# Performance work log

Measured on AMD Instinct MI355X. Metric: run time of the kernel, lower is better.

The kernel has to match this reference:

```python
import jax, jax.numpy as jnp
import numpy as np

K_NEIGHBORS = 16
HEADS = 4
BN_EPS = 1e-5


def _bn(x, p):
    # eval-mode BatchNorm; p is [4, C] = (gamma, beta, running_mean, running_var), x is [..., C]
    g, b, m, v = p[0], p[1], p[2], p[3]
    return (x - m) * (g / jnp.sqrt(v + BN_EPS)) + b


def setup_inputs() -> dict:
    key = jax.random.key(0)
    ks = jax.random.split(key, 16)
    B, C, H, W = 4, 192, 32, 32
    Hd = 384  # hidden_channels

    def bn_params(k, c):
        k1, k2, k3, k4 = jax.random.split(k, 4)
        gamma = 1.0 + 0.1 * jax.random.normal(k1, (c,), jnp.float32)
        beta = 0.1 * jax.random.normal(k2, (c,), jnp.float32)
        mean = 0.1 * jax.random.normal(k3, (c,), jnp.float32)
        var = jax.random.uniform(k4, (c,), jnp.float32, 0.5, 1.5)
        return jnp.stack([gamma, beta, mean, var])

    x = jax.random.normal(ks[0], (B, C, H, W), jnp.float32)
    W1 = 0.05 * jax.random.normal(ks[1], (C, C), jnp.float32)          # fc1 1x1 conv [out,in]
    b1 = 0.02 * jax.random.normal(ks[2], (C,), jnp.float32)
    bn1 = bn_params(ks[3], C)
    Wg = 0.05 * jax.random.normal(ks[4], (C, HEADS * Hd), jnp.float32)  # GATConv shared lin
    att_src = 0.1 * jax.random.normal(ks[5], (HEADS, Hd), jnp.float32)
    att_dst = 0.1 * jax.random.normal(ks[6], (HEADS, Hd), jnp.float32)
    bg = 0.02 * jax.random.normal(ks[7], (Hd,), jnp.float32)            # GATConv bias (concat=False)
    bng = bn_params(ks[8], Hd)
    W2 = 0.05 * jax.random.normal(ks[9], (C, Hd), jnp.float32)          # fc2 1x1 conv [out,in]
    b2 = 0.02 * jax.random.normal(ks[10], (C,), jnp.float32)
    bn2 = bn_params(ks[11], C)
    return {"x": x, "W1": W1, "b1": b1, "bn1": bn1, "Wg": Wg,
            "att_src": att_src, "att_dst": att_dst, "bg": bg, "bng": bng,
            "W2": W2, "b2": b2, "bn2": bn2}


def reference(x, W1, b1, bn1, Wg, att_src, att_dst, bg, bng, W2, b2, bn2):
    B, C, H, W = x.shape
    N = H * W
    Hd = Wg.shape[1] // HEADS
    xf = x.reshape(B, C, N).transpose(0, 2, 1)          # [B,N,C] node features
    shortcut = xf

    # fc1: 1x1 conv + BN
    y = _bn(xf @ W1.T + b1, bn1)                        # [B,N,C]

    # dynamic KNN graph per image (loop=True -> self included, distance 0)
    sq = jnp.sum(y * y, axis=-1)                        # [B,N]
    dist = sq[:, :, None] + sq[:, None, :] - 2.0 * jnp.einsum('bnc,bmc->bnm', y, y)
    idx = jax.lax.top_k(-dist, K_NEIGHBORS)[1]          # [B,N,k] neighbor (source) ids
    bidx = jnp.arange(B)[:, None, None]

    # GATConv (shared lin, heads=4, concat=False -> mean over heads)
    h = (y @ Wg).reshape(B, N, HEADS, Hd)               # [B,N,h,d]
    a_src = jnp.sum(h * att_src, axis=-1)               # [B,N,h]
    a_dst = jnp.sum(h * att_dst, axis=-1)               # [B,N,h]
    e = jax.nn.leaky_relu(a_src[bidx, idx] + a_dst[:, :, None, :], 0.2)  # [B,N,k,h]
    attn = jax.nn.softmax(e, axis=2)                    # softmax over the k incoming edges
    h_nbr = h[bidx, idx]                                # [B,N,k,h,d] gathered neighbor feats
    g = jnp.einsum('bnkh,bnkhd->bnhd', attn, h_nbr).mean(axis=2) + bg  # [B,N,Hd]

    g = jax.nn.gelu(_bn(g, bng), approximate=False)

    # fc2: 1x1 conv + BN, residual
    out = _bn(g @ W2.T + b2, bn2) + shortcut            # [B,N,C]
    return out.transpose(0, 2, 1).reshape(B, C, H, W)
```

## Files before the change

### kernel.cpp

```cpp
#include <hip/hip_runtime.h>
#include <math.h>

#define Bb 4
#define Cc 192
#define NN 1024
#define HD 384
#define NH 4
#define FF 1536
#define KN 16
#define BN_EPS 1e-5f

typedef __attribute__((ext_vector_type(8))) short bf16x8;
typedef __attribute__((ext_vector_type(4))) float f32x4;

__device__ inline float b2f(ushort u) {
  return __uint_as_float(((unsigned)u) << 16);
}
__device__ inline ushort f2b(float f) {
  unsigned v = __float_as_uint(f);
  return (ushort)((v + 0x7fffu + ((v >> 16) & 1u)) >> 16);
}

#define FMA_ROW(ACC, AV, B) \
  ACC.x = fmaf(AV, B.x, ACC.x); ACC.y = fmaf(AV, B.y, ACC.y); \
  ACC.z = fmaf(AV, B.z, ACC.z); ACC.w = fmaf(AV, B.w, ACC.w);

__global__ __launch_bounds__(256) void k_prep(
    const float* __restrict__ W1, const float* __restrict__ W2,
    const float* __restrict__ Wg, float* __restrict__ W1T,
    ushort* __restrict__ W2b, ushort* __restrict__ WgTb) {
  __shared__ float tile[32][33];
  int id = blockIdx.x;
  int t = threadIdx.x;
  if (id < 36 || id >= 108) {
    const float* in; int R, C, cx, cy;
    float* outf = nullptr; ushort* outb = nullptr;
    if (id < 36) { in = W1; R = Cc; C = Cc; cx = id % 6; cy = id / 6; outf = W1T; }
    else { int q = id - 108; in = Wg; R = Cc; C = FF; cx = q % 48; cy = q / 48; outb = WgTb; }
    int c0 = cx * 32, r0 = cy * 32;
    int tx = t & 31, ty = t >> 5;
#pragma unroll
    for (int i = 0; i < 4; ++i) {
      int r = ty + i * 8;
      tile[r][tx] = in[(size_t)(r0 + r) * C + c0 + tx];
    }
    __syncthreads();
#pragma unroll
    for (int i = 0; i < 4; ++i) {
      int r = ty + i * 8;
      float v = tile[tx][r];
      if (outf) outf[(size_t)(c0 + r) * R + r0 + tx] = v;
      else      outb[(size_t)(c0 + r) * R + r0 + tx] = f2b(v);
    }
  } else {
    int base = (id - 36) * 1024 + t * 4;
    float4 v = *(const float4*)&W2[base];
    ushort4 o = {f2b(v.x), f2b(v.y), f2b(v.z), f2b(v.w)};
    *(ushort4*)&W2b[base] = o;
  }
}

__global__ __launch_bounds__(256) void k_fc1(
    const float* __restrict__ x, const float* __restrict__ W1T,
    const float* __restrict__ b1, const float* __restrict__ bn1,
    float* __restrict__ y, ushort* __restrict__ yb,
    float* __restrict__ yT) {
  int nt = blockIdx.x, ct = blockIdx.y, b = blockIdx.z;
  int n0 = nt * 64, ct64 = ct * 64;
  __shared__ float As[64][64];
  __shared__ float Bs[64][64];
  __shared__ float ctile[64][68];
  int t = threadIdx.x;
  int tx = t & 15, ty = t >> 4;
  float4 acc[4];
#pragma unroll
  for (int i = 0; i < 4; ++i) acc[i] = {0.f, 0.f, 0.f, 0.f};
  for (int k0 = 0; k0 < Cc; k0 += 64) {
    __syncthreads();
#pragma unroll
    for (int i = 0; i < 4; ++i) {
      int fi = i * 256 + t;
      int r = fi >> 4, q = fi & 15;
      *(float4*)&As[r][q * 4] =
          *(const float4*)&x[((size_t)b * Cc + k0 + r) * NN + n0 + q * 4];
      *(float4*)&Bs[r][q * 4] =
          *(const float4*)&W1T[(size_t)(k0 + r) * Cc + ct64 + q * 4];
    }
    __syncthreads();
#pragma unroll 8
    for (int k = 0; k < 64; ++k) {
      float4 a = *(const float4*)&As[k][ty * 4];
      float4 bv = *(const float4*)&Bs[k][tx * 4];
      FMA_ROW(acc[0], a.x, bv)
      FMA_ROW(acc[1], a.y, bv)
      FMA_ROW(acc[2], a.z, bv)
      FMA_ROW(acc[3], a.w, bv)
    }
  }
  float s[4], mm[4], be[4], bias[4];
#pragma unroll
  for (int jj = 0; jj < 4; ++jj) {
    int c = ct64 + tx * 4 + jj;
    s[jj]    = bn1[c] / sqrtf(bn1[3 * Cc + c] + BN_EPS);
    mm[jj]   = bn1[2 * Cc + c];
    be[jj]   = bn1[Cc + c];
    bias[jj] = b1[c];
  }
  float accm[4][4] = {
      {acc[0].x, acc[0].y, acc[0].z, acc[0].w},
      {acc[1].x, acc[1].y, acc[1].z, acc[1].w},
      {acc[2].x, acc[2].y, acc[2].z, acc[2].w},
      {acc[3].x, acc[3].y, acc[3].z, acc[3].w}};
#pragma unroll
  for (int ii = 0; ii < 4; ++ii) {
    int n = n0 + ty * 4 + ii;
    float4 o;
    o.x = (accm[ii][0] + bias[0] - mm[0]) * s[0] + be[0];
    o.y = (accm[ii][1] + bias[1] - mm[1]) * s[1] + be[1];
    o.z = (accm[ii][2] + bias[2] - mm[2]) * s[2] + be[2];
    o.w = (accm[ii][3] + bias[3] - mm[3]) * s[3] + be[3];
    *(float4*)&y[((size_t)b * NN + n) * Cc + ct64 + tx * 4] = o;
    ushort4 ob = {f2b(o.x), f2b(o.y), f2b(o.z), f2b(o.w)};
    *(ushort4*)&yb[((size_t)b * NN + n) * Cc + ct64 + tx * 4] = ob;
    ctile[tx * 4 + 0][ty * 4 + ii] = o.x;
    ctile[tx * 4 + 1][ty * 4 + ii] = o.y;
    ctile[tx * 4 + 2][ty * 4 + ii] = o.z;
    ctile[tx * 4 + 3][ty * 4 + ii] = o.w;
  }
  __syncthreads();
#pragma unroll
  for (int i = 0; i < 4; ++i) {
    int u = i * 256 + t;
    int cl = u >> 4, q = u & 15;
    float4 v = *(const float4*)&ctile[cl][q * 4];
    *(float4*)&yT[((size_t)b * Cc + ct64 + cl) * NN + n0 + q * 4] = v;
  }
}

__global__ __launch_bounds__(64) void k_sq(const float* __restrict__ y,
                                           float* __restrict__ sq) {
  int bn = blockIdx.x;
  int lane = threadIdx.x;
  const float* yp = y + (size_t)bn * Cc;
  float s = 0.f;
  for (int k = lane; k < Cc; k += 64) { float v = yp[k]; s = fmaf(v, v, s); }
#pragma unroll
  for (int off = 32; off; off >>= 1) s += __shfl_down(s, off);
  if (lane == 0) sq[bn] = s;
}

__global__ __launch_bounds__(256) void k_hgemm_mfma(
    const ushort* __restrict__ yb, const ushort* __restrict__ WgTb,
    ushort* __restrict__ hb) {
  int r0 = blockIdx.x * 128, c0 = blockIdx.y * 128;
  __shared__ ushort Al[128][72];
  __shared__ ushort Bl[128][72];
  int t = threadIdx.x;
  int w = t >> 6, l = t & 63;
  int wr = w >> 1, wc = w & 1;
  f32x4 acc[4][4];
#pragma unroll
  for (int mt = 0; mt < 4; ++mt)
#pragma unroll
    for (int nt = 0; nt < 4; ++nt) acc[mt][nt] = {0.f, 0.f, 0.f, 0.f};
  for (int k0 = 0; k0 < Cc; k0 += 64) {
    __syncthreads();
#pragma unroll
    for (int i = 0; i < 4; ++i) {
      int u = i * 256 + t;
      int r = u >> 3, ko = (u & 7) * 8;
      *(int4*)&Al[r][ko] = *(const int4*)&yb[(size_t)(r0 + r) * Cc + k0 + ko];
      *(int4*)&Bl[r][ko] = *(const int4*)&WgTb[(size_t)(c0 + r) * Cc + k0 + ko];
    }
    __syncthreads();
#pragma unroll
    for (int ks = 0; ks < 2; ++ks) {
      bf16x8 af[4], bfr[4];
#pragma unroll
      for (int mt = 0; mt < 4; ++mt)
        af[mt] = *(const bf16x8*)&Al[wr * 64 + mt * 16 + (l & 15)][ks * 32 + (l >> 4) * 8];
#pragma unroll
      for (int nt = 0; nt < 4; ++nt)
        bfr[nt] = *(const bf16x8*)&Bl[wc * 64 + nt * 16 + (l & 15)][ks * 32 + (l >> 4) * 8];
#pragma unroll
      for (int mt = 0; mt < 4; ++mt)
#pragma unroll
        for (int nt = 0; nt < 4; ++nt)
          acc[mt][nt] = __builtin_amdgcn_mfma_f32_16x16x32_bf16(
              af[mt], bfr[nt], acc[mt][nt], 0, 0, 0);
    }
  }
  int col_l = l & 15, rg = l >> 4;
#pragma unroll
  for (int mt = 0; mt < 4; ++mt)
#pragma unroll
    for (int nt = 0; nt < 4; ++nt) {
      int col = c0 + wc * 64 + nt * 16 + col_l;
#pragma unroll
      for (int j = 0; j < 4; ++j) {
        int row = r0 + wr * 64 + mt * 16 + rg * 4 + j;
        hb[(size_t)row * FF + col] = f2b(acc[mt][nt][j]);
      }
    }
}

__global__ __launch_bounds__(256) void k_attn_coef(
    const ushort* __restrict__ hb, const float* __restrict__ att_src,
    const float* __restrict__ att_dst, float* __restrict__ asrc,
    float* __restrict__ adst) {
  int bn = blockIdx.x;
  int head = threadIdx.x / 64, lane = threadIdx.x % 64;
  const ushort* hp = hb + (size_t)bn * FF + head * HD;
  const float* as = att_src + head * HD;
  const float* ad = att_dst + head * HD;
  float s1 = 0.f, s2 = 0.f;
  for (int d = lane; d < HD; d += 64) {
    float v = b2f(hp[d]);
    s1 = fmaf(v, as[d], s1);
    s2 = fmaf(v, ad[d], s2);
  }
#pragma unroll
  for (int off = 32; off; off >>= 1) {
    s1 += __shfl_down(s1, off);
    s2 += __shfl_down(s2, off);
  }
  if (lane == 0) {
    asrc[bn * NH + head] = s1;
    adst[bn * NH + head] = s2;
  }
}

__global__ __launch_bounds__(256) void k_dist(const float* __restrict__ yT,
                                              const float* __restrict__ sq,
                                              float* __restrict__ dist) {
  int b = blockIdx.z;
  int n0 = blockIdx.y * 128, m0 = blockIdx.x * 64;
  __shared__ float As[64][128];
  __shared__ float Bs[64][64];
  const float* ytb = yT + (size_t)b * Cc * NN;
  int t = threadIdx.x;
  int tx = t & 15, ty = t >> 4;
  float4 acc[8];
#pragma unroll
  for (int i = 0; i < 8; ++i) acc[i] = {0.f, 0.f, 0.f, 0.f};
  for (int k0 = 0; k0 < Cc; k0 += 64) {
    __syncthreads();
#pragma unroll
    for (int i = 0; i < 8; ++i) {
      int fi = i * 256 + t;
      int kk = fi >> 5, n4 = fi & 31;
      *(float4*)&As[kk][n4 * 4] =
          *(const float4*)&ytb[(size_t)(k0 + kk) * NN + n0 + n4 * 4];
    }
#pragma unroll
    for (int i = 0; i < 4; ++i) {
      int fi = i * 256 + t;
      int kk = fi >> 4, m4 = fi & 15;
      *(float4*)&Bs[kk][m4 * 4] =
          *(const float4*)&ytb[(size_t)(k0 + kk) * NN + m0 + m4 * 4];
    }
    __syncthreads();
#pragma unroll 8
    for (int k = 0; k < 64; ++k) {
      float4 a0 = *(const float4*)&As[k][ty * 4];
      float4 a1 = *(const float4*)&As[k][64 + ty * 4];
      float4 b4 = *(const float4*)&Bs[k][tx * 4];
      FMA_ROW(acc[0], a0.x, b4)
      FMA_ROW(acc[1], a0.y, b4)
      FMA_ROW(acc[2], a0.z, b4)
      FMA_ROW(acc[3], a0.w, b4)
      FMA_ROW(acc[4], a1.x, b4)
      FMA_ROW(acc[5], a1.y, b4)
      FMA_ROW(acc[6], a1.z, b4)
      FMA_ROW(acc[7], a1.w, b4)
    }
  }
#pragma unroll
  for (int ii = 0; ii < 8; ++ii) {
    int n = n0 + ((ii < 4) ? (ty * 4 + ii) : (64 + ty * 4 + ii - 4));
    float sn = sq[b * NN + n];
    int mbase = m0 + tx * 4;
    float av[4] = {acc[ii].x, acc[ii].y, acc[ii].z, acc[ii].w};
    float4 o;
    o.x = sn + sq[b * NN + mbase + 0] - 2.f * av[0];
    o.y = sn + sq[b * NN + mbase + 1] - 2.f * av[1];
    o.z = sn + sq[b * NN + mbase + 2] - 2.f * av[2];
    o.w = sn + sq[b * NN + mbase + 3] - 2.f * av[3];
    *(float4*)&dist[((size_t)b * NN + n) * NN + mbase] = o;
  }
}

__global__ __launch_bounds__(64) void k_topk(const float* __restrict__ dist,
                                             int* __restrict__ idx) {
  int bn = blockIdx.x;
  int lane = threadIdx.x;
  const float4* dp = (const float4*)(dist + (size_t)bn * NN);
  float dv[16];
#pragma unroll
  for (int q = 0; q < 4; ++q) {
    float4 v = dp[lane + 64 * q];
    dv[q * 4 + 0] = v.x; dv[q * 4 + 1] = v.y;
    dv[q * 4 + 2] = v.z; dv[q * 4 + 3] = v.w;
  }
  for (int sel = 0; sel < KN; ++sel) {
    float bv = INFINITY;
    int bi = 0x7fffffff;
#pragma unroll
    for (int q = 0; q < 4; ++q)
#pragma unroll
      for (int j = 0; j < 4; ++j) {
        int m = (lane + 64 * q) * 4 + j;
        float v = dv[q * 4 + j];
        if (v < bv || (v == bv && m < bi)) { bv = v; bi = m; }
      }
#pragma unroll
    for (int off = 32; off; off >>= 1) {
      float ov = __shfl_xor(bv, off);
      int oi   = __shfl_xor(bi, off);
      if (ov < bv || (ov == bv && oi < bi)) { bv = ov; bi = oi; }
    }
    if (lane == 0) idx[bn * KN + sel] = bi;
#pragma unroll
    for (int q = 0; q < 4; ++q)
#pragma unroll
      for (int j = 0; j < 4; ++j)
        if ((lane + 64 * q) * 4 + j == bi) dv[q * 4 + j] = INFINITY;
  }
}

__global__ __launch_bounds__(128, 4) void k_gat(
    const ushort* __restrict__ hb, const float* __restrict__ asrc,
    const float* __restrict__ adst, const int* __restrict__ idx,
    const float* __restrict__ bg, const float* __restrict__ bng,
    ushort* __restrict__ gb) {
  int bid = blockIdx.x;
  int bn = (bid & 7) * (Bb * NN / 8) + (bid >> 3);
  int b = bn / NN;
  __shared__ int nb[KN];
  __shared__ float attn[KN][NH];
  int t = threadIdx.x;
  if (t < KN) nb[t] = idx[bn * KN + t];
  __syncthreads();
  if (t < KN * NH) {
    int k = t % KN, hd = t / KN;
    float e = asrc[((size_t)b * NN + nb[k]) * NH + hd] +
              adst[(size_t)bn * NH + hd];
    e = (e >= 0.f) ? e : 0.2f * e;
    attn[k][hd] = e;
  }
  __syncthreads();
  if (t < NH) {
    float mx = -INFINITY;
    for (int k = 0; k < KN; ++k) mx = fmaxf(mx, attn[k][t]);
    float s = 0.f;
    for (int k = 0; k < KN; ++k) {
      float ev = expf(attn[k][t] - mx);
      attn[k][t] = ev;
      s += ev;
    }
    float inv = 1.f / s;
    for (int k = 0; k < KN; ++k) attn[k][t] *= inv;
  }
  __syncthreads();
  if (t < 96) {
    int d = t * 4;
    float4 acc = {0.f, 0.f, 0.f, 0.f};
#pragma unroll 4
    for (int k = 0; k < KN; ++k) {
      const ushort* hp = hb + ((size_t)b * NN + nb[k]) * FF + d;
      float4 aw = *(const float4*)&attn[k][0];
      ushort4 u0 = *(const ushort4*)&hp[0];
      ushort4 u1 = *(const ushort4*)&hp[HD];
      ushort4 u2 = *(const ushort4*)&hp[2 * HD];
      ushort4 u3 = *(const ushort4*)&hp[3 * HD];
      float4 h0 = {b2f(u0.x), b2f(u0.y), b2f(u0.z), b2f(u0.w)};
      float4 h1 = {b2f(u1.x), b2f(u1.y), b2f(u1.z), b2f(u1.w)};
      float4 h2 = {b2f(u2.x), b2f(u2.y), b2f(u2.z), b2f(u2.w)};
      float4 h3 = {b2f(u3.x), b2f(u3.y), b2f(u3.z), b2f(u3.w)};
      acc.x = fmaf(aw.x, h0.x, acc.x); acc.x = fmaf(aw.y, h1.x, acc.x);
      acc.x = fmaf(aw.z, h2.x, acc.x); acc.x = fmaf(aw.w, h3.x, acc.x);
      acc.y = fmaf(aw.x, h0.y, acc.y); acc.y = fmaf(aw.y, h1.y, acc.y);
      acc.y = fmaf(aw.z, h2.y, acc.y); acc.y = fmaf(aw.w, h3.y, acc.y);
      acc.z = fmaf(aw.x, h0.z, acc.z); acc.z = fmaf(aw.y, h1.z, acc.z);
      acc.z = fmaf(aw.z, h2.z, acc.z); acc.z = fmaf(aw.w, h3.z, acc.z);
      acc.w = fmaf(aw.x, h0.w, acc.w); acc.w = fmaf(aw.y, h1.w, acc.w);
      acc.w = fmaf(aw.z, h2.w, acc.w); acc.w = fmaf(aw.w, h3.w, acc.w);
    }
    float o[4] = {acc.x, acc.y, acc.z, acc.w};
    ushort4 r;
    ushort* rp = (ushort*)&r;
#pragma unroll
    for (int j = 0; j < 4; ++j) {
      int dd = d + j;
      float val = o[j] * 0.25f + bg[dd];
      float sc = bng[dd] / sqrtf(bng[3 * HD + dd] + BN_EPS);
      val = (val - bng[2 * HD + dd]) * sc + bng[HD + dd];
      val = 0.5f * val * (1.f + erff(val * 0.7071067811865475f));
      rp[j] = f2b(val);
    }
    *(ushort4*)&gb[(size_t)bn * HD + d] = r;
  }
}

__global__ __launch_bounds__(256) void k_fc2_mfma(
    const ushort* __restrict__ gb, const ushort* __restrict__ W2b,
    const float* __restrict__ b2, const float* __restrict__ bn2,
    const float* __restrict__ x, float* __restrict__ out) {
  int r0 = blockIdx.x * 64;
  int c0 = blockIdx.y * 64;
  int b = r0 >> 10, n0 = r0 & 1023;
  __shared__ ushort smem[2 * 64 * 72];
  ushort* Al = smem;
  ushort* Bl = smem + 64 * 72;
  int t = threadIdx.x;
  int w = t >> 6, l = t & 63;
  int wr = w >> 1, wc = w & 1;
  f32x4 acc[2][2];
#pragma unroll
  for (int mt = 0; mt < 2; ++mt)
#pragma unroll
    for (int nt = 0; nt < 2; ++nt) acc[mt][nt] = {0.f, 0.f, 0.f, 0.f};
  for (int k0 = 0; k0 < HD; k0 += 64) {
    __syncthreads();
#pragma unroll
    for (int i = 0; i < 2; ++i) {
      int u = i * 256 + t;
      int r = u >> 3, ko = (u & 7) * 8;
      *(int4*)&Al[r * 72 + ko] = *(const int4*)&gb[(size_t)(r0 + r) * HD + k0 + ko];
      *(int4*)&Bl[r * 72 + ko] = *(const int4*)&W2b[(size_t)(c0 + r) * HD + k0 + ko];
    }
    __syncthreads();
#pragma unroll
    for (int ks = 0; ks < 2; ++ks) {
      bf16x8 af[2], bfr[2];
#pragma unroll
      for (int mt = 0; mt < 2; ++mt)
        af[mt] = *(const bf16x8*)&Al[(wr * 32 + mt * 16 + (l & 15)) * 72 + ks * 32 + (l >> 4) * 8];
#pragma unroll
      for (int nt = 0; nt < 2; ++nt)
        bfr[nt] = *(const bf16x8*)&Bl[(wc * 32 + nt * 16 + (l & 15)) * 72 + ks * 32 + (l >> 4) * 8];
#pragma unroll
      for (int mt = 0; mt < 2; ++mt)
#pragma unroll
        for (int nt = 0; nt < 2; ++nt)
          acc[mt][nt] = __builtin_amdgcn_mfma_f32_16x16x32_bf16(
              af[mt], bfr[nt], acc[mt][nt], 0, 0, 0);
    }
  }
  __syncthreads();
  float* ct = (float*)smem;
  int col_l = l & 15, rg = l >> 4;
#pragma unroll
  for (int mt = 0; mt < 2; ++mt)
#pragma unroll
    for (int nt = 0; nt < 2; ++nt) {
      int cl = wc * 32 + nt * 16 + col_l;
      int nl = wr * 32 + mt * 16 + rg * 4;
      float4 v = {acc[mt][nt][0], acc[mt][nt][1], acc[mt][nt][2], acc[mt][nt][3]};
      *(float4*)&ct[cl * 68 + nl] = v;
    }
  __syncthreads();
#pragma unroll
  for (int i = 0; i < 4; ++i) {
    int u = i * 256 + t;
    int cl = u >> 4, q = u & 15;
    float4 v = *(const float4*)&ct[cl * 68 + q * 4];
    int c = c0 + cl;
    float s  = bn2[c] / sqrtf(bn2[3 * Cc + c] + BN_EPS);
    float mm = bn2[2 * Cc + c];
    float be = bn2[Cc + c];
    float bias = b2[c];
    size_t base = ((size_t)b * Cc + c) * NN + n0 + q * 4;
    float4 res = *(const float4*)&x[base];
    float4 o;
    o.x = (v.x + bias - mm) * s + be + res.x;
    o.y = (v.y + bias - mm) * s + be + res.y;
    o.z = (v.z + bias - mm) * s + be + res.z;
    o.w = (v.w + bias - mm) * s + be + res.w;
    *(float4*)&out[base] = o;
  }
}

extern "C" void kernel_launch(void* const* d_in, const int* in_sizes, int n_in,
                              void* d_out, int out_size, void* d_ws, size_t ws_size,
                              hipStream_t stream) {
  const float* x       = (const float*)d_in[0];
  const float* W1      = (const float*)d_in[1];
  const float* b1      = (const float*)d_in[2];
  const float* bn1     = (const float*)d_in[3];
  const float* Wg      = (const float*)d_in[4];
  const float* att_src = (const float*)d_in[5];
  const float* att_dst = (const float*)d_in[6];
  const float* bg      = (const float*)d_in[7];
  const float* bng     = (const float*)d_in[8];
  const float* W2      = (const float*)d_in[9];
  const float* b2      = (const float*)d_in[10];
  const float* bn2     = (const float*)d_in[11];
  float* out = (float*)d_out;

  float* ws    = (float*)d_ws;
  float* y     = ws;
  float* sq    = y + 786432;
  float* asrc  = sq + 4096;
  float* adst  = asrc + 16384;
  float* dist  = adst + 16384;
  int*   idx   = (int*)(dist + 4194304);
  float* yT    = dist + 4194304 + 65536;
  float* W1T   = yT + 786432;
  ushort* yb   = (ushort*)(W1T + 36864);
  ushort* WgTb = yb + 786432;
  ushort* hb   = WgTb + 294912;
  ushort* gb   = hb + 6291456;
  ushort* W2b  = gb + 1572864;

  k_prep<<<396, 256, 0, stream>>>(W1, W2, Wg, W1T, W2b, WgTb);
  k_fc1<<<dim3(16, 3, 4), 256, 0, stream>>>(x, W1T, b1, bn1, y, yb, yT);
  k_sq<<<Bb * NN, 64, 0, stream>>>(y, sq);
  k_hgemm_mfma<<<dim3(32, 12), 256, 0, stream>>>(yb, WgTb, hb);
  k_attn_coef<<<Bb * NN, 256, 0, stream>>>(hb, att_src, att_dst, asrc, adst);
  k_dist<<<dim3(16, 8, 4), 256, 0, stream>>>(yT, sq, dist);
  k_topk<<<Bb * NN, 64, 0, stream>>>(dist, idx);
  k_gat<<<Bb * NN, 128, 0, stream>>>(hb, asrc, adst, idx, bg, bng, gb);
  k_fc2_mfma<<<dim3(64, 3), 256, 0, stream>>>(gb, W2b, b2, bn2, x, out);
}
```

Measured before the change: 133.7 us.

## Fold attention vectors into Wg to compute attention logits from y

Precomputes a small [C,8] matrix Wg·att_src/att_dst per head in the prep kernel. The attention logits then come from y as 8 extra dot products fused into the squared-norm kernel. This removes the separate k_attn_coef kernel, which reread the whole bf16 h tensor. The logits now come from fp32 y and fp32 weights rather than bf16-rounded h, so values differ slightly. The prep blocks use a serial 384-length loop per thread.

```diff
diff --git a/kernel.cpp b/kernel.cpp
--- a/kernel.cpp
+++ b/kernel.cpp
@@ -27,12 +27,14 @@
 
 __global__ __launch_bounds__(256) void k_prep(
     const float* __restrict__ W1, const float* __restrict__ W2,
-    const float* __restrict__ Wg, float* __restrict__ W1T,
-    ushort* __restrict__ W2b, ushort* __restrict__ WgTb) {
+    const float* __restrict__ Wg, const float* __restrict__ att_src,
+    const float* __restrict__ att_dst, float* __restrict__ W1T,
+    ushort* __restrict__ W2b, ushort* __restrict__ WgTb,
+    float* __restrict__ Asml) {
   __shared__ float tile[32][33];
   int id = blockIdx.x;
   int t = threadIdx.x;
-  if (id < 36 || id >= 108) {
+  if (id < 36 || (id >= 108 && id < 396)) {
     const float* in; int R, C, cx, cy;
     float* outf = nullptr; ushort* outb = nullptr;
     if (id < 36) { in = W1; R = Cc; C = Cc; cx = id % 6; cy = id / 6; outf = W1T; }
@@ -52,11 +54,20 @@
       if (outf) outf[(size_t)(c0 + r) * R + r0 + tx] = v;
       else      outb[(size_t)(c0 + r) * R + r0 + tx] = f2b(v);
     }
-  } else {
+  } else if (id < 108) {
     int base = (id - 36) * 1024 + t * 4;
     float4 v = *(const float4*)&W2[base];
     ushort4 o = {f2b(v.x), f2b(v.y), f2b(v.z), f2b(v.w)};
     *(ushort4*)&W2b[base] = o;
+  } else {
+    int gi = (id - 396) * 256 + t;
+    int k = gi >> 3, j = gi & 7;
+    int h = j & 3;
+    const float* av = (j < 4) ? att_src : att_dst;
+    float acc = 0.f;
+    for (int d = 0; d < HD; ++d)
+      acc = fmaf(Wg[(size_t)k * FF + h * HD + d], av[h * HD + d], acc);
+    Asml[k * 8 + j] = acc;
   }
 }
 
@@ -137,16 +148,40 @@
   }
 }
 
-__global__ __launch_bounds__(64) void k_sq(const float* __restrict__ y,
-                                           float* __restrict__ sq) {
+__global__ __launch_bounds__(64) void k_sqatt(
+    const float* __restrict__ y, const float* __restrict__ Asml,
+    float* __restrict__ sq, float* __restrict__ asrc,
+    float* __restrict__ adst) {
   int bn = blockIdx.x;
   int lane = threadIdx.x;
   const float* yp = y + (size_t)bn * Cc;
   float s = 0.f;
-  for (int k = lane; k < Cc; k += 64) { float v = yp[k]; s = fmaf(v, v, s); }
-#pragma unroll
-  for (int off = 32; off; off >>= 1) s += __shfl_down(s, off);
-  if (lane == 0) sq[bn] = s;
+  float p[8] = {0.f, 0.f, 0.f, 0.f, 0.f, 0.f, 0.f, 0.f};
+#pragma unroll
+  for (int i = 0; i < 3; ++i) {
+    int k = lane + i * 64;
+    float v = yp[k];
+    s = fmaf(v, v, s);
+    float4 a0 = *(const float4*)&Asml[k * 8];
+    float4 a1 = *(const float4*)&Asml[k * 8 + 4];
+    p[0] = fmaf(v, a0.x, p[0]); p[1] = fmaf(v, a0.y, p[1]);
+    p[2] = fmaf(v, a0.z, p[2]); p[3] = fmaf(v, a0.w, p[3]);
+    p[4] = fmaf(v, a1.x, p[4]); p[5] = fmaf(v, a1.y, p[5]);
+    p[6] = fmaf(v, a1.z, p[6]); p[7] = fmaf(v, a1.w, p[7]);
+  }
+#pragma unroll
+  for (int off = 32; off; off >>= 1) {
+    s += __shfl_down(s, off);
+#pragma unroll
+    for (int j = 0; j < 8; ++j) p[j] += __shfl_down(p[j], off);
+  }
+  if (lane == 0) {
+    sq[bn] = s;
+    float4 o1 = {p[0], p[1], p[2], p[3]};
+    float4 o2 = {p[4], p[5], p[6], p[7]};
+    *(float4*)&asrc[bn * NH] = o1;
+    *(float4*)&adst[bn * NH] = o2;
+  }
 }
 
 __global__ __launch_bounds__(256) void k_hgemm_mfma(
@@ -202,32 +237,6 @@
         hb[(size_t)row * FF + col] = f2b(acc[mt][nt][j]);
       }
     }
-}
-
-__global__ __launch_bounds__(256) void k_attn_coef(
-    const ushort* __restrict__ hb, const float* __restrict__ att_src,
-    const float* __restrict__ att_dst, float* __restrict__ asrc,
-    float* __restrict__ adst) {
-  int bn = blockIdx.x;
-  int head = threadIdx.x / 64, lane = threadIdx.x % 64;
-  const ushort* hp = hb + (size_t)bn * FF + head * HD;
-  const float* as = att_src + head * HD;
-  const float* ad = att_dst + head * HD;
-  float s1 = 0.f, s2 = 0.f;
-  for (int d = lane; d < HD; d += 64) {
-    float v = b2f(hp[d]);
-    s1 = fmaf(v, as[d], s1);
-    s2 = fmaf(v, ad[d], s2);
-  }
-#pragma unroll
-  for (int off = 32; off; off >>= 1) {
-    s1 += __shfl_down(s1, off);
-    s2 += __shfl_down(s2, off);
-  }
-  if (lane == 0) {
-    asrc[bn * NH + head] = s1;
-    adst[bn * NH + head] = s2;
-  }
 }
 
 __global__ __launch_bounds__(256) void k_dist(const float* __restrict__ yT,
@@ -507,17 +516,17 @@
   int*   idx   = (int*)(dist + 4194304);
   float* yT    = dist + 4194304 + 65536;
   float* W1T   = yT + 786432;
-  ushort* yb   = (ushort*)(W1T + 36864);
+  float* Asml  = W1T + 36864;
+  ushort* yb   = (ushort*)(Asml + 1536);
   ushort* WgTb = yb + 786432;
   ushort* hb   = WgTb + 294912;
   ushort* gb   = hb + 6291456;
   ushort* W2b  = gb + 1572864;
 
-  k_prep<<<396, 256, 0, stream>>>(W1, W2, Wg, W1T, W2b, WgTb);
+  k_prep<<<402, 256, 0, stream>>>(W1, W2, Wg, att_src, att_dst, W1T, W2b, WgTb, Asml);
   k_fc1<<<dim3(16, 3, 4), 256, 0, stream>>>(x, W1T, b1, bn1, y, yb, yT);
-  k_sq<<<Bb * NN, 64, 0, stream>>>(y, sq);
+  k_sqatt<<<Bb * NN, 64, 0, stream>>>(y, Asml, sq, asrc, adst);
   k_hgemm_mfma<<<dim3(32, 12), 256, 0, stream>>>(yb, WgTb, hb);
-  k_attn_coef<<<Bb * NN, 256, 0, stream>>>(hb, att_src, att_dst, asrc, adst);
   k_dist<<<dim3(16, 8, 4), 256, 0, stream>>>(yT, sq, dist);
   k_topk<<<Bb * NN, 64, 0, stream>>>(dist, idx);
   k_gat<<<Bb * NN, 128, 0, stream>>>(hb, asrc, adst, idx, bg, bng, gb);
```

New measurement: 141.6 us. +5.9%, slower.
